# Kernel optimization log

Measured on AMD Instinct MI355X. Metric: run time of the kernel, lower is better.

The kernel has to match this reference:

```python
import jax, jax.numpy as jnp
import numpy as np

NTYPES = 2
MAXNEI = 128      # maxNeighborNum
M2 = 16
NPER = 256        # atoms per type
B = 4
EMB = [25, 50, 100]
FIT_IN = M2 * EMB[-1]  # 1600
FH = 240


def setup_inputs() -> dict:
    key = jax.random.key(0)
    ks = jax.random.split(key, 16)
    s = 0.1
    inp = {
        "Ri": jax.random.normal(ks[0], (B, NTYPES * NPER, NTYPES * MAXNEI, 4), jnp.float32),
        "emb_W0": jax.random.normal(ks[1], (4, 1, EMB[0]), jnp.float32) * s,
        "emb_b0": jax.random.normal(ks[2], (4, EMB[0]), jnp.float32) * s,
        "emb_W1": jax.random.normal(ks[3], (4, EMB[0], EMB[1]), jnp.float32) * s,
        "emb_b1": jax.random.normal(ks[4], (4, EMB[1]), jnp.float32) * s,
        "emb_W2": jax.random.normal(ks[5], (4, EMB[1], EMB[2]), jnp.float32) * s,
        "emb_b2": jax.random.normal(ks[6], (4, EMB[2]), jnp.float32) * s,
        "fit_W0": jax.random.normal(ks[7], (2, FIT_IN, FH), jnp.float32) * 0.02,
        "fit_b0": jax.random.normal(ks[8], (2, FH), jnp.float32) * s,
        "fit_W1": jax.random.normal(ks[9], (2, FH, FH), jnp.float32) * 0.05,
        "fit_b1": jax.random.normal(ks[10], (2, FH), jnp.float32) * s,
        "fit_W2": jax.random.normal(ks[11], (2, FH, FH), jnp.float32) * 0.05,
        "fit_b2": jax.random.normal(ks[12], (2, FH), jnp.float32) * s,
        "fit_W3": jax.random.normal(ks[13], (2, FH, 1), jnp.float32) * 0.05,
        "fit_b3": jax.random.normal(ks[14], (2, 1), jnp.float32),
    }
    return inp


def _emb(s, W0, b0, W1, b1, W2, b2):
    # DeepMD-style embedding MLP with doubling resnet skips (1->25->50->100)
    h0 = jnp.tanh(s @ W0 + b0)
    h1 = jnp.tanh(h0 @ W1 + b1) + jnp.concatenate([h0, h0], axis=-1)
    h2 = jnp.tanh(h1 @ W2 + b2) + jnp.concatenate([h1, h1], axis=-1)
    return h2


def _fit(d, W0, b0, W1, b1, W2, b2, W3, b3):
    h = jnp.tanh(d @ W0 + b0)
    h = jnp.tanh(h @ W1 + b1) + h   # resnet skip (equal dims)
    h = jnp.tanh(h @ W2 + b2) + h
    return h @ W3 + b3              # [B, N, 1]


def reference(Ri, emb_W0, emb_b0, emb_W1, emb_b1, emb_W2, emb_b2,
              fit_W0, fit_b0, fit_W1, fit_b1, fit_W2, fit_b2, fit_W3, fit_b3):
    type_nums = NTYPES
    Ei_blocks = []
    for i in range(NTYPES):                      # center-atom type
        Ri_i = Ri[:, i * NPER:(i + 1) * NPER]    # [B, NPER, NTYPES*M, 4]
        xyz = None
        for j in range(NTYPES):                  # neighbor type
            blk = Ri_i[:, :, j * MAXNEI:(j + 1) * MAXNEI, :]  # [B,N,M,4]
            S = blk[..., 0:1]                                  # [B,N,M,1]
            e = i * NTYPES + j
            G = _emb(S, emb_W0[e], emb_b0[e], emb_W1[e], emb_b1[e],
                     emb_W2[e], emb_b2[e])                     # [B,N,M,100]
            tmp = jnp.einsum('bnmc,bnmg->bncg', blk, G)        # [B,N,4,100]
            xyz = tmp if xyz is None else xyz + tmp
        xyz = xyz / (MAXNEI * type_nums)
        xyz_b = xyz[..., :M2]                                  # [B,N,4,16]
        DR = jnp.einsum('bncg,bnch->bngh', xyz, xyz_b)         # [B,N,100,16]
        DR = DR.reshape(B, NPER, FIT_IN)
        Ei_i = _fit(DR, fit_W0[i], fit_b0[i], fit_W1[i], fit_b1[i],
                    fit_W2[i], fit_b2[i], fit_W3[i], fit_b3[i])  # [B,N,1]
        Ei_blocks.append(Ei_i)
    Ei = jnp.concatenate(Ei_blocks, axis=1)     # [B, natoms_sum, 1]
    return Ei[..., 0]                            # per-atom energies [B, natoms_sum]
```

## Files before the change

### kernel.cpp

```cpp
#include <hip/hip_runtime.h>
#include <hip/hip_bf16.h>

#define FH 240
#define FIT_IN 1600
#define NK 2048
#define TLO -16.0f
#define TINVH 64.0f
#define KSPLIT0 17
#define CHUNK0 96

typedef _Float16 h8 __attribute__((ext_vector_type(8)));
typedef float f4v __attribute__((ext_vector_type(4)));

__device__ __forceinline__ float fast_tanh(float x) {
    float e2 = __builtin_amdgcn_exp2f(x * 2.8853900817779268f);
    return 1.0f - 2.0f * __builtin_amdgcn_rcpf(e2 + 1.0f);
}

#define FMA_ROW(r, s) \
    acc[r][0] += (s) * b0.x; acc[r][1] += (s) * b0.y; \
    acc[r][2] += (s) * b0.z; acc[r][3] += (s) * b0.w; \
    acc[r][4] += (s) * b1.x; acc[r][5] += (s) * b1.y; \
    acc[r][6] += (s) * b1.z; acc[r][7] += (s) * b1.w;

#define TOFF_W0   0
#define TOFF_B0   28
#define TOFF_B1   56
#define TOFF_B2   108
#define TOFF_W1   208
#define TOFF_W2   1508
#define TOFF_H0T  6708
#define TOFF_H1T  10008
#define TSMEM     16608

__global__ __launch_bounds__(256) void k_prep(
    const float* __restrict__ eW0, const float* __restrict__ eB0,
    const float* __restrict__ eW1, const float* __restrict__ eB1,
    const float* __restrict__ eW2, const float* __restrict__ eB2,
    float* __restrict__ T,
    const float* __restrict__ fW0, const float* __restrict__ fW1,
    const float* __restrict__ fW2,
    _Float16* __restrict__ W0T, _Float16* __restrict__ W1T,
    _Float16* __restrict__ W2T)
{
    __shared__ float sm[TSMEM];
    const int t = threadIdx.x;

    if (blockIdx.x >= 64) {
        const int bid0 = blockIdx.x - 64;
        const int total = 768000 + 115200 + 115200;
        for (int idx = bid0 * 256 + t; idx < total; idx += 448 * 256) {
            if (idx < 768000) {
                const int tp = idx / 384000, r = idx - tp * 384000;
                const int n = r / 1600, k = r - n * 1600;
                W0T[idx] = (_Float16)fW0[tp * 384000 + k * 240 + n];
            } else if (idx < 883200) {
                const int j = idx - 768000;
                const int tp = j / 57600, r = j - tp * 57600;
                const int n = r / 240, k = r - n * 240;
                W1T[j] = (_Float16)fW1[tp * 57600 + k * 240 + n];
            } else {
                const int j = idx - 883200;
                const int tp = j / 57600, r = j - tp * 57600;
                const int n = r / 240, k = r - n * 240;
                W2T[j] = (_Float16)fW2[tp * 57600 + k * 240 + n];
            }
        }
        return;
    }

    const int w    = t >> 6;
    const int lane = t & 63;
    const int mi   = lane & 7;
    const int gi   = lane >> 3;
    const int mrow = w * 32 + mi * 4;

    const int e  = blockIdx.x >> 4;
    const int k0 = (blockIdx.x & 15) * 128;

    for (int idx = t; idx < 1250; idx += 256) {
        int k = idx / 50, g = idx - k * 50;
        sm[TOFF_W1 + k * 52 + g] = eW1[e * 1250 + idx];
    }
    for (int idx = t; idx < 5000; idx += 256) {
        int k = idx / 100, r = idx - k * 100;
        int half = r / 50, g = r - half * 50;
        sm[TOFF_W2 + k * 104 + half * 52 + g] = eW2[e * 5000 + idx];
    }
    if (t < 25)       { sm[TOFF_W0 + t] = eW0[e * 25 + t]; sm[TOFF_B0 + t] = eB0[e * 25 + t]; }
    else if (t < 75)  { sm[TOFF_B1 + (t - 25)] = eB1[e * 50 + (t - 25)]; }
    else if (t < 175) { sm[TOFF_B2 + (t - 75)] = eB2[e * 100 + (t - 75)]; }
    __syncthreads();

    if (t < 128) {
        const float S = TLO + (float)(k0 + t) * (1.0f / TINVH);
        #pragma unroll
        for (int k = 0; k < 25; ++k)
            sm[TOFF_H0T + k * 132 + t] = fast_tanh(S * sm[TOFF_W0 + k] + sm[TOFF_B0 + k]);
    }
    __syncthreads();

    {
        float acc[4][8];
        #pragma unroll
        for (int r = 0; r < 4; ++r)
            #pragma unroll
            for (int c = 0; c < 8; ++c) acc[r][c] = 0.f;

        #pragma unroll 5
        for (int k = 0; k < 25; ++k) {
            const float4 av = *(const float4*)&sm[TOFF_H0T + k * 132 + mrow];
            const float4 b0 = *(const float4*)&sm[TOFF_W1 + k * 52 + gi * 8];
            const float4 b1 = *(const float4*)&sm[TOFF_W1 + k * 52 + gi * 8 + 4];
            FMA_ROW(0, av.x) FMA_ROW(1, av.y) FMA_ROW(2, av.z) FMA_ROW(3, av.w)
        }
        #pragma unroll
        for (int c = 0; c < 8; ++c) {
            const int g = gi * 8 + c;
            if (g < 50) {
                const int gm = (g < 25) ? g : g - 25;
                const float4 h0r = *(const float4*)&sm[TOFF_H0T + gm * 132 + mrow];
                const float bias = sm[TOFF_B1 + g];
                float4 o;
                o.x = fast_tanh(acc[0][c] + bias) + h0r.x;
                o.y = fast_tanh(acc[1][c] + bias) + h0r.y;
                o.z = fast_tanh(acc[2][c] + bias) + h0r.z;
                o.w = fast_tanh(acc[3][c] + bias) + h0r.w;
                *(float4*)&sm[TOFF_H1T + g * 132 + mrow] = o;
            }
        }
    }
    __syncthreads();

    for (int half = 0; half < 2; ++half) {
        float acc[4][8];
        #pragma unroll
        for (int r = 0; r < 4; ++r)
            #pragma unroll
            for (int c = 0; c < 8; ++c) acc[r][c] = 0.f;

        #pragma unroll 5
        for (int k = 0; k < 50; ++k) {
            const float4 av = *(const float4*)&sm[TOFF_H1T + k * 132 + mrow];
            const float4 b0 = *(const float4*)&sm[TOFF_W2 + k * 104 + half * 52 + gi * 8];
            const float4 b1 = *(const float4*)&sm[TOFF_W2 + k * 104 + half * 52 + gi * 8 + 4];
            FMA_ROW(0, av.x) FMA_ROW(1, av.y) FMA_ROW(2, av.z) FMA_ROW(3, av.w)
        }
        #pragma unroll
        for (int c = 0; c < 8; ++c) {
            const int g = gi * 8 + c;
            if (g < 50) {
                const float4 h1r = *(const float4*)&sm[TOFF_H1T + g * 132 + mrow];
                const float bias = sm[TOFF_B2 + half * 50 + g];
                float* out = T + ((size_t)e * NK + k0 + mrow) * 100 + half * 50 + g;
                out[0]   = fast_tanh(acc[0][c] + bias) + h1r.x;
                out[100] = fast_tanh(acc[1][c] + bias) + h1r.y;
                out[200] = fast_tanh(acc[2][c] + bias) + h1r.z;
                out[300] = fast_tanh(acc[3][c] + bias) + h1r.w;
            }
        }
    }
}

__global__ __launch_bounds__(256) void k_xyz(
    const float* __restrict__ Ri, const float* __restrict__ T,
    _Float16* __restrict__ DRh)
{
    __shared__ float4 sR[256];
    __shared__ float  sF[256];
    __shared__ int    sI[256];
    __shared__ float  sXYZ[400];

    const int t   = threadIdx.x;
    const int blk = blockIdx.x;
    const int b   = blk >> 9;
    const int i   = (blk >> 8) & 1;
    const int n   = blk & 255;

    for (int idx = t; idx < 400; idx += 256) sXYZ[idx] = 0.f;

    {
        const int jj = t >> 7, m = t & 127;
        const size_t row = ((size_t)(b * 512 + i * 256 + n)) * 256 + jj * 128 + m;
        const float4 r = *(const float4*)(Ri + row * 4);
        sR[t] = r;
        float u = (r.x - TLO) * TINVH;
        int ii = (int)u;
        ii = (ii < 0) ? 0 : ((ii > NK - 2) ? NK - 2 : ii);
        sI[t] = ii;
        sF[t] = u - (float)ii;
    }
    __syncthreads();

    const int jj = t >> 7;
    const int g  = t & 127;
    if (g < 100) {
        const float* Te = T + ((size_t)(i * 2 + jj)) * NK * 100 + g;
        float a0 = 0.f, a1 = 0.f, a2 = 0.f, a3 = 0.f;
        #pragma unroll 4
        for (int m = 0; m < 128; ++m) {
            const int s = jj * 128 + m;
            const float4 R = sR[s];
            const float  f = sF[s];
            const float* p = Te + (size_t)sI[s] * 100;
            const float v0 = p[0], v1 = p[100];
            const float G = v0 + f * (v1 - v0);
            a0 += R.x * G; a1 += R.y * G; a2 += R.z * G; a3 += R.w * G;
        }
        atomicAdd(&sXYZ[g],       a0);
        atomicAdd(&sXYZ[100 + g], a1);
        atomicAdd(&sXYZ[200 + g], a2);
        atomicAdd(&sXYZ[300 + g], a3);
    }
    __syncthreads();

    const float inv = 1.0f / 65536.0f;
    _Float16* dr = DRh + (((size_t)i * 4 + b) * 256 + n) * FIT_IN;
    for (int q = t; q < 400; q += 256) {
        const int gg = q >> 2, h0 = (q & 3) * 4;
        ushort4 pk;
        _Float16* ph = (_Float16*)&pk;
        #pragma unroll
        for (int r = 0; r < 4; ++r) {
            const int h = h0 + r;
            const float v = (sXYZ[gg] * sXYZ[h] + sXYZ[100 + gg] * sXYZ[100 + h]
                           + sXYZ[200 + gg] * sXYZ[200 + h] + sXYZ[300 + gg] * sXYZ[300 + h]) * inv;
            ph[r] = (_Float16)v;
        }
        *(ushort4*)(dr + gg * 16 + h0) = pk;
    }
}

__global__ __launch_bounds__(256) void k_fit_mfma(
    const _Float16* __restrict__ A, const _Float16* __restrict__ WT,
    float* __restrict__ P)
{
    __shared__ _Float16 sW[240 * 104];
    __shared__ _Float16 sA[64 * 104];

    const int t    = threadIdx.x;
    const int w    = t >> 6;
    const int lane = t & 63;
    const int ln   = lane & 15;
    const int quad = lane >> 4;

    const int mtile = blockIdx.x;
    const int ks    = blockIdx.y;
    const int row0  = mtile * 64;
    const int tp    = mtile >> 4;
    const int kbeg  = ks * CHUNK0;
    const int kend  = (kbeg + CHUNK0 < FIT_IN) ? (kbeg + CHUNK0) : FIT_IN;
    const int klen  = kend - kbeg;
    const int nf0   = w * 4;
    const int nfrags = (w < 3) ? 4 : 3;

    const _Float16* Ab = A + (size_t)row0 * FIT_IN + kbeg;
    const _Float16* Wb = WT + (size_t)tp * 240 * FIT_IN + kbeg;

    for (int q = t; q < 240 * 24; q += 256) {
        const int n = q / 24, kq = (q - n * 24) * 4;
        if (kq < klen)
            *(uint2*)&sW[n * 104 + kq] = *(const uint2*)(Wb + (size_t)n * FIT_IN + kq);
    }
    for (int q = t; q < 64 * 24; q += 256) {
        const int m = q / 24, kq = (q - m * 24) * 4;
        if (kq < klen)
            *(uint2*)&sA[m * 104 + kq] = *(const uint2*)(Ab + (size_t)m * FIT_IN + kq);
    }
    __syncthreads();

    f4v acc[4][4];
    #pragma unroll
    for (int mf = 0; mf < 4; ++mf)
        #pragma unroll
        for (int nf = 0; nf < 4; ++nf) acc[mf][nf] = (f4v)0.f;

    for (int k0 = 0; k0 < klen; k0 += 32) {
        h8 afr[4];
        #pragma unroll
        for (int mf = 0; mf < 4; ++mf)
            afr[mf] = *(const h8*)&sA[(mf * 16 + ln) * 104 + k0 + quad * 8];
        #pragma unroll
        for (int nf = 0; nf < 4; ++nf) {
            if (nf < nfrags) {
                const h8 bfr = *(const h8*)&sW[((nf0 + nf) * 16 + ln) * 104 + k0 + quad * 8];
                #pragma unroll
                for (int mf = 0; mf < 4; ++mf)
                    acc[mf][nf] = __builtin_amdgcn_mfma_f32_16x16x32_f16(
                        afr[mf], bfr, acc[mf][nf], 0, 0, 0);
            }
        }
    }

    float* Pb = P + ((size_t)ks * 2048 + row0) * FH;
    #pragma unroll
    for (int nf = 0; nf < 4; ++nf) {
        if (nf < nfrags) {
            const int col = (nf0 + nf) * 16 + ln;
            #pragma unroll
            for (int mf = 0; mf < 4; ++mf)
                #pragma unroll
                for (int r = 0; r < 4; ++r) {
                    const int row = mf * 16 + quad * 4 + r;
                    Pb[(size_t)row * FH + col] = acc[mf][nf][r];
                }
        }
    }
}

__global__ __launch_bounds__(256) void k_fit_tail(
    const float* __restrict__ P,
    const _Float16* __restrict__ W1T, const _Float16* __restrict__ W2T,
    const float* __restrict__ fb0, const float* __restrict__ fb1,
    const float* __restrict__ fb2, const float* __restrict__ fW3,
    const float* __restrict__ fb3, float* __restrict__ out)
{
    __shared__ _Float16 sStage[64 * 248];
    __shared__ _Float16 sAbuf[2][16 * 264];
    __shared__ float    hRes[16 * 240];

    const int t    = threadIdx.x;
    const int w    = t >> 6;
    const int lane = t & 63;
    const int ln   = lane & 15;
    const int quad = lane >> 4;
    const int r0   = blockIdx.x * 16;
    const int tp   = r0 >> 10;

    for (int q = t; q < 2 * 16 * 264; q += 256) ((_Float16*)sAbuf)[q] = (_Float16)0.f;
    if (t < 128) {
        const int n = t >> 1, kq = 240 + (t & 1) * 4;
        *(uint2*)&sStage[n * 248 + kq] = make_uint2(0u, 0u);
    }

    #pragma unroll
    for (int j = 0; j < 15; ++j) {
        const int e = t + j * 256;
        const int m = e / 240, col = e - m * 240;
        const size_t base = (size_t)(r0 + m) * FH + col;
        float s = 0.f;
        #pragma unroll
        for (int ks = 0; ks < KSPLIT0; ++ks)
            s += P[(size_t)ks * 2048 * FH + base];
        const float v = fast_tanh(s + fb0[tp * FH + col]);
        hRes[m * 240 + col] = v;
        sAbuf[0][m * 264 + col] = (_Float16)v;
    }

    for (int layer = 0; layer < 2; ++layer) {
        const _Float16* Wt = (layer == 0 ? W1T : W2T) + (size_t)tp * FH * FH;
        const float* Bias  = (layer == 0 ? fb1 : fb2) + tp * FH;
        const _Float16* inA = sAbuf[layer];
        _Float16* outA      = sAbuf[layer ^ 1];

        for (int p = 0; p < 4; ++p) {
            __syncthreads();
            const int nrows = (p < 3) ? 64 : 48;
            for (int q = t; q < 64 * 60; q += 256) {
                const int n = q / 60, kq = (q - n * 60) * 4;
                if (n < nrows)
                    *(uint2*)&sStage[n * 248 + kq] =
                        *(const uint2*)(Wt + (size_t)(p * 64 + n) * FH + kq);
            }
            __syncthreads();

            const int f = p * 4 + w;
            if (f < 15) {
                f4v acc = (f4v)0.f;
                #pragma unroll
                for (int s = 0; s < 8; ++s) {
                    const h8 afr = *(const h8*)&inA[ln * 264 + s * 32 + quad * 8];
                    const h8 bfr = *(const h8*)&sStage[(w * 16 + ln) * 248 + s * 32 + quad * 8];
                    acc = __builtin_amdgcn_mfma_f32_16x16x32_f16(afr, bfr, acc, 0, 0, 0);
                }
                const int col = f * 16 + ln;
                const float bias = Bias[col];
                #pragma unroll
                for (int r = 0; r < 4; ++r) {
                    const int m = quad * 4 + r;
                    const float v = fast_tanh(acc[r] + bias) + hRes[m * 240 + col];
                    hRes[m * 240 + col] = v;
                    outA[m * 264 + col] = (_Float16)v;
                }
            }
        }
    }
    __syncthreads();

    const float* wv = fW3 + tp * FH;
    #pragma unroll
    for (int rr = 0; rr < 4; ++rr) {
        const int m = w * 4 + rr;
        float s = 0.f;
        for (int k = lane; k < FH; k += 64)
            s += hRes[m * 240 + k] * wv[k];
        #pragma unroll
        for (int off = 32; off > 0; off >>= 1) s += __shfl_down(s, off);
        if (lane == 0) {
            const int gr = r0 + m;
            const int b = (gr >> 8) & 3, n = gr & 255;
            out[b * 512 + tp * 256 + n] = s + fb3[tp];
        }
    }
}

extern "C" void kernel_launch(void* const* d_in, const int* in_sizes, int n_in,
                              void* d_out, int out_size, void* d_ws, size_t ws_size,
                              hipStream_t stream)
{
    const float* Ri  = (const float*)d_in[0];
    const float* eW0 = (const float*)d_in[1];
    const float* eB0 = (const float*)d_in[2];
    const float* eW1 = (const float*)d_in[3];
    const float* eB1 = (const float*)d_in[4];
    const float* eW2 = (const float*)d_in[5];
    const float* eB2 = (const float*)d_in[6];
    const float* fW0 = (const float*)d_in[7];
    const float* fb0 = (const float*)d_in[8];
    const float* fW1 = (const float*)d_in[9];
    const float* fb1 = (const float*)d_in[10];
    const float* fW2 = (const float*)d_in[11];
    const float* fb2 = (const float*)d_in[12];
    const float* fW3 = (const float*)d_in[13];
    const float* fb3 = (const float*)d_in[14];

    char* p = (char*)d_ws;
    float* T   = (float*)p;                 p += (size_t)4 * NK * 100 * 4;
    float* P   = (float*)p;                 p += (size_t)KSPLIT0 * 2048 * FH * 4;
    _Float16* DRh = (_Float16*)p;           p += (size_t)2048 * FIT_IN * 2;
    _Float16* W0T = (_Float16*)p;           p += (size_t)768000 * 2;
    _Float16* W1T = (_Float16*)p;           p += (size_t)115200 * 2;
    _Float16* W2T = (_Float16*)p;           p += (size_t)115200 * 2;

    k_prep<<<dim3(512), dim3(256), 0, stream>>>(eW0, eB0, eW1, eB1, eW2, eB2, T,
                                                fW0, fW1, fW2, W0T, W1T, W2T);
    k_xyz<<<dim3(2048), dim3(256), 0, stream>>>(Ri, T, DRh);

    k_fit_mfma<<<dim3(32, KSPLIT0), dim3(256), 0, stream>>>(DRh, W0T, P);

    k_fit_tail<<<dim3(128), dim3(256), 0, stream>>>(P, W1T, W2T, fb0, fb1, fb2, fW3, fb3,
                                                    (float*)d_out);
}
```

Baseline: 213.4 us.

## Replace split-K first fit layer with full-K N-tiled MFMA kernel fusing bias+tanh

The first fitting layer no longer splits K into 17 chunks that write fp32 partial sums later reduced by the tail kernel. Each block now owns a 64-row by 16-column output tile over the full 1600-wide K. It stages that weight slice in LDS, streams A fragments straight from global memory with a 4-deep register prefetch, and applies bias and tanh in the epilogue. This removes the large partial-sum buffer and its write and read-back traffic. In exchange each block has a long serial MFMA chain with a single accumulator, and A rows are reread by 15 column blocks.

```diff
diff --git a/kernel.cpp b/kernel.cpp
--- a/kernel.cpp
+++ b/kernel.cpp
@@ -6,8 +6,6 @@
 #define NK 2048
 #define TLO -16.0f
 #define TINVH 64.0f
-#define KSPLIT0 17
-#define CHUNK0 96
 
 typedef _Float16 h8 __attribute__((ext_vector_type(8)));
 typedef float f4v __attribute__((ext_vector_type(4)));
@@ -231,12 +229,11 @@
     }
 }
 
-__global__ __launch_bounds__(256) void k_fit_mfma(
-    const _Float16* __restrict__ A, const _Float16* __restrict__ WT,
-    float* __restrict__ P)
+__global__ __launch_bounds__(256) void k_fit0(
+    const _Float16* __restrict__ DRh, const _Float16* __restrict__ W0T,
+    const float* __restrict__ fb0, float* __restrict__ hA)
 {
-    __shared__ _Float16 sW[240 * 104];
-    __shared__ _Float16 sA[64 * 104];
+    __shared__ _Float16 sW[16 * 1608];
 
     const int t    = threadIdx.x;
     const int w    = t >> 6;
@@ -244,76 +241,53 @@
     const int ln   = lane & 15;
     const int quad = lane >> 4;
 
-    const int mtile = blockIdx.x;
-    const int ks    = blockIdx.y;
-    const int row0  = mtile * 64;
-    const int tp    = mtile >> 4;
-    const int kbeg  = ks * CHUNK0;
-    const int kend  = (kbeg + CHUNK0 < FIT_IN) ? (kbeg + CHUNK0) : FIT_IN;
-    const int klen  = kend - kbeg;
-    const int nf0   = w * 4;
-    const int nfrags = (w < 3) ? 4 : 3;
-
-    const _Float16* Ab = A + (size_t)row0 * FIT_IN + kbeg;
-    const _Float16* Wb = WT + (size_t)tp * 240 * FIT_IN + kbeg;
-
-    for (int q = t; q < 240 * 24; q += 256) {
-        const int n = q / 24, kq = (q - n * 24) * 4;
-        if (kq < klen)
-            *(uint2*)&sW[n * 104 + kq] = *(const uint2*)(Wb + (size_t)n * FIT_IN + kq);
-    }
-    for (int q = t; q < 64 * 24; q += 256) {
-        const int m = q / 24, kq = (q - m * 24) * 4;
-        if (kq < klen)
-            *(uint2*)&sA[m * 104 + kq] = *(const uint2*)(Ab + (size_t)m * FIT_IN + kq);
-    }
-    __syncthreads();
-
-    f4v acc[4][4];
+    const int m  = blockIdx.x;
+    const int nt = blockIdx.y;
+    const int r0 = m * 64;
+    const int tp = m >> 4;
+    const int n0 = nt * 16;
+
+    const _Float16* Wb = W0T + ((size_t)tp * 240 + n0) * FIT_IN;
+    for (int q = t; q < 6400; q += 256) {
+        const int row = q / 400, kq = (q - row * 400) * 4;
+        *(uint2*)&sW[row * 1608 + kq] = *(const uint2*)(Wb + (size_t)row * FIT_IN + kq);
+    }
+    __syncthreads();
+
+    const int rw = r0 + w * 16;
+    const _Float16* A0 = DRh + (size_t)(rw + ln) * FIT_IN;
+    const int kq = quad * 8;
+
+    f4v acc = (f4v)0.f;
+    h8 p0 = *(const h8*)(A0 + 0 * 32 + kq);
+    h8 p1 = *(const h8*)(A0 + 1 * 32 + kq);
+    h8 p2 = *(const h8*)(A0 + 2 * 32 + kq);
+    h8 p3 = *(const h8*)(A0 + 3 * 32 + kq);
+
+    #pragma unroll 4
+    for (int s = 0; s < 50; ++s) {
+        h8 pf = p3;
+        if (s + 4 < 50) pf = *(const h8*)(A0 + (s + 4) * 32 + kq);
+        const h8 bfr = *(const h8*)&sW[ln * 1608 + s * 32 + kq];
+        acc = __builtin_amdgcn_mfma_f32_16x16x32_f16(p0, bfr, acc, 0, 0, 0);
+        p0 = p1; p1 = p2; p2 = p3; p3 = pf;
+    }
+
+    const int col  = n0 + ln;
+    const float bias = fb0[tp * FH + col];
     #pragma unroll
-    for (int mf = 0; mf < 4; ++mf)
-        #pragma unroll
-        for (int nf = 0; nf < 4; ++nf) acc[mf][nf] = (f4v)0.f;
-
-    for (int k0 = 0; k0 < klen; k0 += 32) {
-        h8 afr[4];
-        #pragma unroll
-        for (int mf = 0; mf < 4; ++mf)
-            afr[mf] = *(const h8*)&sA[(mf * 16 + ln) * 104 + k0 + quad * 8];
-        #pragma unroll
-        for (int nf = 0; nf < 4; ++nf) {
-            if (nf < nfrags) {
-                const h8 bfr = *(const h8*)&sW[((nf0 + nf) * 16 + ln) * 104 + k0 + quad * 8];
-                #pragma unroll
-                for (int mf = 0; mf < 4; ++mf)
-                    acc[mf][nf] = __builtin_amdgcn_mfma_f32_16x16x32_f16(
-                        afr[mf], bfr, acc[mf][nf], 0, 0, 0);
-            }
-        }
-    }
-
-    float* Pb = P + ((size_t)ks * 2048 + row0) * FH;
-    #pragma unroll
-    for (int nf = 0; nf < 4; ++nf) {
-        if (nf < nfrags) {
-            const int col = (nf0 + nf) * 16 + ln;
-            #pragma unroll
-            for (int mf = 0; mf < 4; ++mf)
-                #pragma unroll
-                for (int r = 0; r < 4; ++r) {
-                    const int row = mf * 16 + quad * 4 + r;
-                    Pb[(size_t)row * FH + col] = acc[mf][nf][r];
-                }
-        }
+    for (int r = 0; r < 4; ++r) {
+        const int row = rw + quad * 4 + r;
+        hA[(size_t)row * FH + col] = fast_tanh(acc[r] + bias);
     }
 }
 
 __global__ __launch_bounds__(256) void k_fit_tail(
-    const float* __restrict__ P,
+    const float* __restrict__ hA,
     const _Float16* __restrict__ W1T, const _Float16* __restrict__ W2T,
-    const float* __restrict__ fb0, const float* __restrict__ fb1,
-    const float* __restrict__ fb2, const float* __restrict__ fW3,
-    const float* __restrict__ fb3, float* __restrict__ out)
+    const float* __restrict__ fb1, const float* __restrict__ fb2,
+    const float* __restrict__ fW3, const float* __restrict__ fb3,
+    float* __restrict__ out)
 {
     __shared__ _Float16 sStage[64 * 248];
     __shared__ _Float16 sAbuf[2][16 * 264];
@@ -337,12 +311,7 @@
     for (int j = 0; j < 15; ++j) {
         const int e = t + j * 256;
         const int m = e / 240, col = e - m * 240;
-        const size_t base = (size_t)(r0 + m) * FH + col;
-        float s = 0.f;
-        #pragma unroll
-        for (int ks = 0; ks < KSPLIT0; ++ks)
-            s += P[(size_t)ks * 2048 * FH + base];
-        const float v = fast_tanh(s + fb0[tp * FH + col]);
+        const float v = hA[(size_t)r0 * FH + e];
         hRes[m * 240 + col] = v;
         sAbuf[0][m * 264 + col] = (_Float16)v;
     }
@@ -426,18 +395,18 @@
 
     char* p = (char*)d_ws;
     float* T   = (float*)p;                 p += (size_t)4 * NK * 100 * 4;
-    float* P   = (float*)p;                 p += (size_t)KSPLIT0 * 2048 * FH * 4;
     _Float16* DRh = (_Float16*)p;           p += (size_t)2048 * FIT_IN * 2;
     _Float16* W0T = (_Float16*)p;           p += (size_t)768000 * 2;
     _Float16* W1T = (_Float16*)p;           p += (size_t)115200 * 2;
     _Float16* W2T = (_Float16*)p;           p += (size_t)115200 * 2;
+    float* hA  = (float*)p;                 p += (size_t)2048 * FH * 4;
 
     k_prep<<<dim3(512), dim3(256), 0, stream>>>(eW0, eB0, eW1, eB1, eW2, eB2, T,
                                                 fW0, fW1, fW2, W0T, W1T, W2T);
     k_xyz<<<dim3(2048), dim3(256), 0, stream>>>(Ri, T, DRh);
 
-    k_fit_mfma<<<dim3(32, KSPLIT0), dim3(256), 0, stream>>>(DRh, W0T, P);
-
-    k_fit_tail<<<dim3(128), dim3(256), 0, stream>>>(P, W1T, W2T, fb0, fb1, fb2, fW3, fb3,
-                                                    (float*)d_out);
-}
+    k_fit0<<<dim3(32, 15), dim3(256), 0, stream>>>(DRh, W0T, fb0, hA);
+
+    k_fit_tail<<<dim3(128), dim3(256), 0, stream>>>(hA, W1T, W2T, fb1, fb2,
+                                                    fW3, fb3, (float*)d_out);
+}
```

Measured after the change: 200.0 us. 6.3% less time.

## Stream K tiles through small LDS buffers in fit GEMM and halve split-K

Applied to the files above, without the earlier changes.

The first fitting-layer GEMM now loads A and W0 in 32-wide K slices per iteration into small shared buffers, with barriers around each slice, instead of staging a whole 96-wide chunk up front. Split-K drops from 17 to 8 with 200-wide chunks, so fewer partial sums are written to and reduced from P. The tail kernel's weight staging now issues all global loads into registers before writing shared memory, with clamped row indices, to overlap load latency. Risks: per-slice sync without double buffering exposes load latency, and fewer blocks (256) lowers occupancy across the GPU.

```diff
diff --git a/kernel.cpp b/kernel.cpp
--- a/kernel.cpp
+++ b/kernel.cpp
@@ -6,8 +6,8 @@
 #define NK 2048
 #define TLO -16.0f
 #define TINVH 64.0f
-#define KSPLIT0 17
-#define CHUNK0 96
+#define KSPLIT0 8
+#define CHUNK0 200
 
 typedef _Float16 h8 __attribute__((ext_vector_type(8)));
 typedef float f4v __attribute__((ext_vector_type(4)));
@@ -231,12 +231,13 @@
     }
 }
 
+template<int K, int CHUNK>
 __global__ __launch_bounds__(256) void k_fit_mfma(
     const _Float16* __restrict__ A, const _Float16* __restrict__ WT,
     float* __restrict__ P)
 {
-    __shared__ _Float16 sW[240 * 104];
-    __shared__ _Float16 sA[64 * 104];
+    __shared__ _Float16 sA[64 * 40];
+    __shared__ _Float16 sBT[240 * 40];
 
     const int t    = threadIdx.x;
     const int w    = t >> 6;
@@ -248,26 +249,10 @@
     const int ks    = blockIdx.y;
     const int row0  = mtile * 64;
     const int tp    = mtile >> 4;
-    const int kbeg  = ks * CHUNK0;
-    const int kend  = (kbeg + CHUNK0 < FIT_IN) ? (kbeg + CHUNK0) : FIT_IN;
-    const int klen  = kend - kbeg;
+    const int kbeg  = ks * CHUNK;
+    const int kend  = (kbeg + CHUNK < K) ? (kbeg + CHUNK) : K;
     const int nf0   = w * 4;
     const int nfrags = (w < 3) ? 4 : 3;
-
-    const _Float16* Ab = A + (size_t)row0 * FIT_IN + kbeg;
-    const _Float16* Wb = WT + (size_t)tp * 240 * FIT_IN + kbeg;
-
-    for (int q = t; q < 240 * 24; q += 256) {
-        const int n = q / 24, kq = (q - n * 24) * 4;
-        if (kq < klen)
-            *(uint2*)&sW[n * 104 + kq] = *(const uint2*)(Wb + (size_t)n * FIT_IN + kq);
-    }
-    for (int q = t; q < 64 * 24; q += 256) {
-        const int m = q / 24, kq = (q - m * 24) * 4;
-        if (kq < klen)
-            *(uint2*)&sA[m * 104 + kq] = *(const uint2*)(Ab + (size_t)m * FIT_IN + kq);
-    }
-    __syncthreads();
 
     f4v acc[4][4];
     #pragma unroll
@@ -275,21 +260,42 @@
         #pragma unroll
         for (int nf = 0; nf < 4; ++nf) acc[mf][nf] = (f4v)0.f;
 
-    for (int k0 = 0; k0 < klen; k0 += 32) {
+    const _Float16* Ab = A + (size_t)row0 * K;
+    const _Float16* Wb = WT + (size_t)tp * 240 * K;
+
+    for (int k0 = kbeg; k0 < kend; k0 += 32) {
+        #pragma unroll
+        for (int q = t; q < 512; q += 256) {
+            const int m = q >> 3, kq = (q & 7) * 4;
+            const int k = k0 + kq;
+            uint2 v = make_uint2(0u, 0u);
+            if (k < kend) v = *(const uint2*)(Ab + (size_t)m * K + k);
+            *(uint2*)&sA[m * 40 + kq] = v;
+        }
+        for (int q = t; q < 1920; q += 256) {
+            const int n = q >> 3, kq = (q & 7) * 4;
+            const int k = k0 + kq;
+            uint2 v = make_uint2(0u, 0u);
+            if (k < kend) v = *(const uint2*)(Wb + (size_t)n * K + k);
+            *(uint2*)&sBT[n * 40 + kq] = v;
+        }
+        __syncthreads();
+
         h8 afr[4];
         #pragma unroll
         for (int mf = 0; mf < 4; ++mf)
-            afr[mf] = *(const h8*)&sA[(mf * 16 + ln) * 104 + k0 + quad * 8];
+            afr[mf] = *(const h8*)&sA[(mf * 16 + ln) * 40 + quad * 8];
         #pragma unroll
         for (int nf = 0; nf < 4; ++nf) {
             if (nf < nfrags) {
-                const h8 bfr = *(const h8*)&sW[((nf0 + nf) * 16 + ln) * 104 + k0 + quad * 8];
+                const h8 bfr = *(const h8*)&sBT[((nf0 + nf) * 16 + ln) * 40 + quad * 8];
                 #pragma unroll
                 for (int mf = 0; mf < 4; ++mf)
                     acc[mf][nf] = __builtin_amdgcn_mfma_f32_16x16x32_f16(
                         afr[mf], bfr, acc[mf][nf], 0, 0, 0);
             }
         }
+        __syncthreads();
     }
 
     float* Pb = P + ((size_t)ks * 2048 + row0) * FH;
@@ -355,12 +361,20 @@
 
         for (int p = 0; p < 4; ++p) {
             __syncthreads();
-            const int nrows = (p < 3) ? 64 : 48;
-            for (int q = t; q < 64 * 60; q += 256) {
+            const int rmax = (p < 3) ? 63 : 47;
+            uint2 ld[15];
+            #pragma unroll
+            for (int j = 0; j < 15; ++j) {
+                const int q = t + j * 256;
                 const int n = q / 60, kq = (q - n * 60) * 4;
-                if (n < nrows)
-                    *(uint2*)&sStage[n * 248 + kq] =
-                        *(const uint2*)(Wt + (size_t)(p * 64 + n) * FH + kq);
+                const int nc = (n > rmax) ? rmax : n;
+                ld[j] = *(const uint2*)(Wt + (size_t)(p * 64 + nc) * FH + kq);
+            }
+            #pragma unroll
+            for (int j = 0; j < 15; ++j) {
+                const int q = t + j * 256;
+                const int n = q / 60, kq = (q - n * 60) * 4;
+                *(uint2*)&sStage[n * 248 + kq] = ld[j];
             }
             __syncthreads();
 
@@ -436,7 +450,7 @@
                                                 fW0, fW1, fW2, W0T, W1T, W2T);
     k_xyz<<<dim3(2048), dim3(256), 0, stream>>>(Ri, T, DRh);
 
-    k_fit_mfma<<<dim3(32, KSPLIT0), dim3(256), 0, stream>>>(DRh, W0T, P);
+    k_fit_mfma<FIT_IN, CHUNK0><<<dim3(32, KSPLIT0), dim3(256), 0, stream>>>(DRh, W0T, P);
 
     k_fit_tail<<<dim3(128), dim3(256), 0, stream>>>(P, W1T, W2T, fb0, fb1, fb2, fW3, fb3,
                                                     (float*)d_out);
```

After: 173.9 us. -18.5%, faster.
